# Optimization experiments

Hardware: AMD Instinct MI355X
Metric: run time of the kernel (lower is better)

The kernel has to match this reference:

```python
import jax, jax.numpy as jnp
import numpy as np

HIDDEN = 128
TEMP = 1.0


def setup_inputs() -> dict:
    key = jax.random.key(0)
    k1, k2, k3, k4, k5, k6 = jax.random.split(key, 6)
    N, D = 524288, 256
    num_segments = 2048
    x = jax.random.normal(k1, (N, D), dtype=jnp.float32)
    segment_ids = jnp.sort(jax.random.randint(k2, (N,), 0, num_segments)).astype(jnp.int32)
    # MLP params: Linear(D,128) -> Tanh -> Linear(128,1)
    s1 = 1.0 / np.sqrt(D)
    s2 = 1.0 / np.sqrt(HIDDEN)
    W1 = jax.random.uniform(k3, (D, HIDDEN), jnp.float32, -s1, s1)
    b1 = jax.random.uniform(k4, (HIDDEN,), jnp.float32, -s1, s1)
    W2 = jax.random.uniform(k5, (HIDDEN, 1), jnp.float32, -s2, s2)
    b2 = jax.random.uniform(k6, (1,), jnp.float32, -s2, s2)
    return {"x": x, "segment_ids": segment_ids, "num_segments": num_segments,
            "W1": W1, "b1": b1, "W2": W2, "b2": b2}


def reference(x, segment_ids, num_segments, W1, b1, W2, b2):
    # per-token attention logit: [N, 1]
    h = jnp.tanh(x @ W1 + b1)
    logits = h @ W2 + b2  # [N, 1]
    z = (logits / TEMP)[:, 0]  # [N]
    # segment-wise numerically-stable softmax
    seg_max = jax.ops.segment_max(z, segment_ids, num_segments=num_segments)  # [S]
    e = jnp.exp(z - seg_max[segment_ids])  # [N]
    seg_sum = jax.ops.segment_sum(e, segment_ids, num_segments=num_segments)  # [S]
    attn_weights = (e / seg_sum[segment_ids])[:, None]  # [N, 1]
    # weighted sum per segment -> [S, D]
    context_vectors = jax.ops.segment_sum(attn_weights * x, segment_ids,
                                          num_segments=num_segments)
    return (context_vectors, attn_weights)
```

## Files before the change

kernel.cpp:

```cpp
#include <hip/hip_runtime.h>

#define D 256
#define H 128
#define CHUNK 32
#define PAD_LD 260

typedef __attribute__((ext_vector_type(8))) short bf16x8;
typedef __attribute__((ext_vector_type(4))) float f32x4;

__device__ __forceinline__ short f2bf(float f) {
    union { float f; unsigned u; } v; v.f = f;
    unsigned r = v.u + 0x7FFFu + ((v.u >> 16) & 1u);
    return (short)(r >> 16);
}

__device__ __forceinline__ float fast_tanh(float a) {
    float t = __expf(2.0f * a);
    return (t - 1.0f) / (t + 1.0f);
}

__global__ __launch_bounds__(256)
void attn_pool_kernel(const float* __restrict__ x, const int* __restrict__ ids,
                      const float* __restrict__ W1, const float* __restrict__ b1,
                      const float* __restrict__ W2, const float* __restrict__ b2,
                      float* __restrict__ ctx_out, float* __restrict__ attn_out,
                      int N)
{
    const int seg  = blockIdx.x;
    const int tid  = threadIdx.x;
    const int lane = tid & 63;
    const int wave = tid >> 6;
    const int q    = lane >> 4;
    const int ln   = lane & 15;

    __shared__ float xs[CHUNK][PAD_LD];
    __shared__ float zpart[CHUNK];

    int lo = 0, hi = N;
    while (lo < hi) { int mid = (lo + hi) >> 1; if (ids[mid] < seg) lo = mid + 1; else hi = mid; }
    const int start = lo;
    hi = N;
    while (lo < hi) { int mid = (lo + hi) >> 1; if (ids[mid] < seg + 1) lo = mid + 1; else hi = mid; }
    const int end = lo;
    const int len = end - start;

    if (len == 0) {
        ctx_out[seg * D + tid] = 0.0f;
        return;
    }

    const int c0 = wave * 32 + ln;
    const int c1 = c0 + 16;
    bf16x8 bfrag[2][8];
#pragma unroll
    for (int s = 0; s < 8; ++s) {
        const int kbase = s * 32 + q * 8;
        bf16x8 f0, f1;
#pragma unroll
        for (int j = 0; j < 8; ++j) {
            f0[j] = f2bf(W1[(kbase + j) * H + c0]);
            f1[j] = f2bf(W1[(kbase + j) * H + c1]);
        }
        bfrag[0][s] = f0; bfrag[1][s] = f1;
    }
    const float b1v0 = b1[c0], b1v1 = b1[c1];
    const float w2v0 = W2[c0], w2v1 = W2[c1];
    const float b2v  = b2[0];

    float m_run = -__builtin_inff();
    float l_run = 0.0f;
    float c_acc = 0.0f;

    const float* xseg  = x + (size_t)start * D;
    float*       zglob = attn_out + start;

    const int nchunks = (len + CHUNK - 1) / CHUNK;
    for (int ch = 0; ch < nchunks; ++ch) {
        const int rbase = ch * CHUNK;
        const int valid = min(CHUNK, len - rbase);

        if (tid < CHUNK) zpart[tid] = 0.0f;
#pragma unroll
        for (int it = 0; it < 8; ++it) {
            const int e   = it * 1024 + tid * 4;
            const int r   = e >> 8;
            const int col = e & 255;
            float4 v = make_float4(0.0f, 0.0f, 0.0f, 0.0f);
            if (r < valid) v = *(const float4*)(xseg + (size_t)(rbase + r) * D + col);
            *(float4*)&xs[r][col] = v;
        }
        __syncthreads();

        f32x4 acc[2][2];
#pragma unroll
        for (int mt = 0; mt < 2; ++mt)
#pragma unroll
            for (int nt = 0; nt < 2; ++nt)
                acc[mt][nt] = (f32x4){0.0f, 0.0f, 0.0f, 0.0f};
#pragma unroll
        for (int s = 0; s < 8; ++s) {
            const int k0 = s * 32 + q * 8;
            const float* p0 = &xs[ln][k0];
            const float* p1 = &xs[16 + ln][k0];
            bf16x8 a0, a1;
#pragma unroll
            for (int j = 0; j < 8; ++j) { a0[j] = f2bf(p0[j]); a1[j] = f2bf(p1[j]); }
            acc[0][0] = __builtin_amdgcn_mfma_f32_16x16x32_bf16(a0, bfrag[0][s], acc[0][0], 0, 0, 0);
            acc[0][1] = __builtin_amdgcn_mfma_f32_16x16x32_bf16(a0, bfrag[1][s], acc[0][1], 0, 0, 0);
            acc[1][0] = __builtin_amdgcn_mfma_f32_16x16x32_bf16(a1, bfrag[0][s], acc[1][0], 0, 0, 0);
            acc[1][1] = __builtin_amdgcn_mfma_f32_16x16x32_bf16(a1, bfrag[1][s], acc[1][1], 0, 0, 0);
        }

#pragma unroll
        for (int mt = 0; mt < 2; ++mt) {
            float v[4];
#pragma unroll
            for (int r = 0; r < 4; ++r) {
                const float h0 = fast_tanh(acc[mt][0][r] + b1v0);
                const float h1 = fast_tanh(acc[mt][1][r] + b1v1);
                v[r] = h0 * w2v0 + h1 * w2v1;
            }
#pragma unroll
            for (int off = 8; off >= 1; off >>= 1)
#pragma unroll
                for (int r = 0; r < 4; ++r)
                    v[r] += __shfl_xor(v[r], off, 16);
            if (ln == 0) {
#pragma unroll
                for (int r = 0; r < 4; ++r)
                    atomicAdd(&zpart[mt * 16 + q * 4 + r], v[r]);
            }
        }
        __syncthreads();

        float cmax = -__builtin_inff();
        for (int r = 0; r < valid; ++r) cmax = fmaxf(cmax, zpart[r]);
        cmax += b2v;
        const float new_m = fmaxf(m_run, cmax);
        const float alpha = __expf(m_run - new_m);
        float lsum = 0.0f, csum = 0.0f;
        for (int r = 0; r < valid; ++r) {
            const float e = __expf(zpart[r] + b2v - new_m);
            lsum += e;
            csum += e * xs[r][tid];
        }
        c_acc = c_acc * alpha + csum;
        l_run = l_run * alpha + lsum;
        m_run = new_m;

        if (tid < valid) zglob[rbase + tid] = zpart[tid] + b2v;
        __syncthreads();
    }

    const float inv = 1.0f / l_run;
    ctx_out[seg * D + tid] = c_acc * inv;
    for (int i = tid; i < len; i += 256) {
        const float zi = zglob[i];
        zglob[i] = __expf(zi - m_run) * inv;
    }
}

extern "C" void kernel_launch(void* const* d_in, const int* in_sizes, int n_in,
                              void* d_out, int out_size, void* d_ws, size_t ws_size,
                              hipStream_t stream) {
    const float* x   = (const float*)d_in[0];
    const int*   ids = (const int*)d_in[1];
    const float* W1  = (const float*)d_in[3];
    const float* b1  = (const float*)d_in[4];
    const float* W2  = (const float*)d_in[5];
    const float* b2  = (const float*)d_in[6];

    const int N = in_sizes[0] / D;
    const int S = (out_size - N) / D;
    float* ctx  = (float*)d_out;
    float* attn = (float*)d_out + (size_t)S * D;

    attn_pool_kernel<<<S, 256, 0, stream>>>(x, ids, W1, b1, W2, b2, ctx, attn, N);
}
```

Baseline: 847.8 us.

## Stage x as bf16 in LDS, parallelize softmax reduction, re-read x for context

Each x chunk is converted to bf16 once while staging it into LDS, so MFMA A-fragments become single vector loads instead of per-element conversions. The shared-memory atomics on per-row logits are replaced by per-wave partial buffers, and the per-chunk max and sum are computed with a 32-lane shuffle reduction instead of every thread looping serially. The context accumulation now re-reads fp32 x from global memory (expected to hit cache) with float4 per thread over a row subset, then reduces across waves through LDS at the end. The smaller LDS footprint and the occupancy hint in launch_bounds aim for more resident blocks, at the cost of a second read of x and extra synchronisation.

```diff
diff --git a/kernel.cpp b/kernel.cpp
--- a/kernel.cpp
+++ b/kernel.cpp
@@ -3,7 +3,7 @@
 #define D 256
 #define H 128
 #define CHUNK 32
-#define PAD_LD 260
+#define PADB 264
 
 typedef __attribute__((ext_vector_type(8))) short bf16x8;
 typedef __attribute__((ext_vector_type(4))) float f32x4;
@@ -19,7 +19,7 @@
     return (t - 1.0f) / (t + 1.0f);
 }
 
-__global__ __launch_bounds__(256)
+__global__ __launch_bounds__(256, 4)
 void attn_pool_kernel(const float* __restrict__ x, const int* __restrict__ ids,
                       const float* __restrict__ W1, const float* __restrict__ b1,
                       const float* __restrict__ W2, const float* __restrict__ b2,
@@ -33,16 +33,18 @@
     const int q    = lane >> 4;
     const int ln   = lane & 15;
 
-    __shared__ float xs[CHUNK][PAD_LD];
-    __shared__ float zpart[CHUNK];
+    __shared__ short xs_bf[CHUNK][PADB];
+    __shared__ float zw[4][CHUNK];
+    __shared__ float ez[CHUNK];
+    __shared__ float bc[2];
+    __shared__ float ctxbuf[4][64][4];
 
     int lo = 0, hi = N;
     while (lo < hi) { int mid = (lo + hi) >> 1; if (ids[mid] < seg) lo = mid + 1; else hi = mid; }
     const int start = lo;
     hi = N;
     while (lo < hi) { int mid = (lo + hi) >> 1; if (ids[mid] < seg + 1) lo = mid + 1; else hi = mid; }
-    const int end = lo;
-    const int len = end - start;
+    const int len = lo - start;
 
     if (len == 0) {
         ctx_out[seg * D + tid] = 0.0f;
@@ -67,27 +69,30 @@
     const float w2v0 = W2[c0], w2v1 = W2[c1];
     const float b2v  = b2[0];
 
-    float m_run = -__builtin_inff();
-    float l_run = 0.0f;
-    float c_acc = 0.0f;
+    float  m_run = -__builtin_inff();
+    float  l_run = 0.0f;
+    float4 c_acc = make_float4(0.0f, 0.0f, 0.0f, 0.0f);
 
     const float* xseg  = x + (size_t)start * D;
     float*       zglob = attn_out + start;
+
+    const int sr = wave;
+    const int sc = (tid & 63) * 4;
 
     const int nchunks = (len + CHUNK - 1) / CHUNK;
     for (int ch = 0; ch < nchunks; ++ch) {
         const int rbase = ch * CHUNK;
         const int valid = min(CHUNK, len - rbase);
-
-        if (tid < CHUNK) zpart[tid] = 0.0f;
+        const float* gsrc = xseg + (size_t)rbase * D;
+
 #pragma unroll
         for (int it = 0; it < 8; ++it) {
-            const int e   = it * 1024 + tid * 4;
-            const int r   = e >> 8;
-            const int col = e & 255;
+            const int r = it * 4 + sr;
             float4 v = make_float4(0.0f, 0.0f, 0.0f, 0.0f);
-            if (r < valid) v = *(const float4*)(xseg + (size_t)(rbase + r) * D + col);
-            *(float4*)&xs[r][col] = v;
+            if (r < valid) v = *(const float4*)(gsrc + (size_t)r * D + sc);
+            short4 b;
+            b.x = f2bf(v.x); b.y = f2bf(v.y); b.z = f2bf(v.z); b.w = f2bf(v.w);
+            *(short4*)&xs_bf[r][sc] = b;
         }
         __syncthreads();
 
@@ -97,14 +102,12 @@
 #pragma unroll
             for (int nt = 0; nt < 2; ++nt)
                 acc[mt][nt] = (f32x4){0.0f, 0.0f, 0.0f, 0.0f};
+        const short* a0p = &xs_bf[ln][q * 8];
+        const short* a1p = &xs_bf[16 + ln][q * 8];
 #pragma unroll
         for (int s = 0; s < 8; ++s) {
-            const int k0 = s * 32 + q * 8;
-            const float* p0 = &xs[ln][k0];
-            const float* p1 = &xs[16 + ln][k0];
-            bf16x8 a0, a1;
-#pragma unroll
-            for (int j = 0; j < 8; ++j) { a0[j] = f2bf(p0[j]); a1[j] = f2bf(p1[j]); }
+            const bf16x8 a0 = *(const bf16x8*)(a0p + s * 32);
+            const bf16x8 a1 = *(const bf16x8*)(a1p + s * 32);
             acc[0][0] = __builtin_amdgcn_mfma_f32_16x16x32_bf16(a0, bfrag[0][s], acc[0][0], 0, 0, 0);
             acc[0][1] = __builtin_amdgcn_mfma_f32_16x16x32_bf16(a0, bfrag[1][s], acc[0][1], 0, 0, 0);
             acc[1][0] = __builtin_amdgcn_mfma_f32_16x16x32_bf16(a1, bfrag[0][s], acc[1][0], 0, 0, 0);
@@ -128,35 +131,65 @@
             if (ln == 0) {
 #pragma unroll
                 for (int r = 0; r < 4; ++r)
-                    atomicAdd(&zpart[mt * 16 + q * 4 + r], v[r]);
+                    zw[wave][mt * 16 + q * 4 + r] = v[r];
             }
         }
         __syncthreads();
 
-        float cmax = -__builtin_inff();
-        for (int r = 0; r < valid; ++r) cmax = fmaxf(cmax, zpart[r]);
-        cmax += b2v;
-        const float new_m = fmaxf(m_run, cmax);
-        const float alpha = __expf(m_run - new_m);
-        float lsum = 0.0f, csum = 0.0f;
-        for (int r = 0; r < valid; ++r) {
-            const float e = __expf(zpart[r] + b2v - new_m);
-            lsum += e;
-            csum += e * xs[r][tid];
-        }
-        c_acc = c_acc * alpha + csum;
-        l_run = l_run * alpha + lsum;
-        m_run = new_m;
-
-        if (tid < valid) zglob[rbase + tid] = zpart[tid] + b2v;
+        if (tid < CHUNK) {
+            const float zz = zw[0][tid] + zw[1][tid] + zw[2][tid] + zw[3][tid] + b2v;
+            float zm = (tid < valid) ? zz : -__builtin_inff();
+            float mx = zm;
+#pragma unroll
+            for (int off = 16; off >= 1; off >>= 1)
+                mx = fmaxf(mx, __shfl_xor(mx, off, 32));
+            const float nm = fmaxf(m_run, mx);
+            const float e  = (tid < valid) ? __expf(zm - nm) : 0.0f;
+            ez[tid] = e;
+            float ls = e;
+#pragma unroll
+            for (int off = 16; off >= 1; off >>= 1)
+                ls += __shfl_xor(ls, off, 32);
+            if (tid == 0) { bc[0] = nm; bc[1] = ls; }
+            if (tid < valid) zglob[rbase + tid] = zz;
+        }
+        __syncthreads();
+
+        const float nm    = bc[0];
+        const float ls    = bc[1];
+        const float alpha = __expf(m_run - nm);
+        m_run = nm;
+        l_run = l_run * alpha + ls;
+        c_acc.x *= alpha; c_acc.y *= alpha; c_acc.z *= alpha; c_acc.w *= alpha;
+#pragma unroll
+        for (int it = 0; it < 8; ++it) {
+            const int r = it * 4 + sr;
+            if (r < valid) {
+                const float  e = ez[r];
+                const float4 v = *(const float4*)(gsrc + (size_t)r * D + sc);
+                c_acc.x += e * v.x; c_acc.y += e * v.y;
+                c_acc.z += e * v.z; c_acc.w += e * v.w;
+            }
+        }
         __syncthreads();
     }
 
     const float inv = 1.0f / l_run;
-    ctx_out[seg * D + tid] = c_acc * inv;
+    ctxbuf[sr][tid & 63][0] = c_acc.x * inv;
+    ctxbuf[sr][tid & 63][1] = c_acc.y * inv;
+    ctxbuf[sr][tid & 63][2] = c_acc.z * inv;
+    ctxbuf[sr][tid & 63][3] = c_acc.w * inv;
+    __syncthreads();
+    if (tid < 64) {
+        float4 s;
+        s.x = ctxbuf[0][tid][0] + ctxbuf[1][tid][0] + ctxbuf[2][tid][0] + ctxbuf[3][tid][0];
+        s.y = ctxbuf[0][tid][1] + ctxbuf[1][tid][1] + ctxbuf[2][tid][1] + ctxbuf[3][tid][1];
+        s.z = ctxbuf[0][tid][2] + ctxbuf[1][tid][2] + ctxbuf[2][tid][2] + ctxbuf[3][tid][2];
+        s.w = ctxbuf[0][tid][3] + ctxbuf[1][tid][3] + ctxbuf[2][tid][3] + ctxbuf[3][tid][3];
+        *(float4*)&ctx_out[seg * D + tid * 4] = s;
+    }
     for (int i = tid; i < len; i += 256) {
-        const float zi = zglob[i];
-        zglob[i] = __expf(zi - m_run) * inv;
+        zglob[i] = __expf(zglob[i] - m_run) * inv;
     }
 }
 
```

Measured after the change: 786.3 us. 7.3% less time.
